# Performance work log

Hardware: AMD Instinct MI355X
Metric: run time of the kernel (lower is better)

Reference implementation:

```python
import jax, jax.numpy as jnp
import numpy as np

B, SP, SH, H, E, V, C = 128, 128, 64, 1024, 300, 50000, 4


def setup_inputs() -> dict:
    key = jax.random.key(0)
    ks = jax.random.split(key, 21)
    def n(k, shape, sc=0.05):
        return sc * jax.random.normal(k, shape, dtype=jnp.float32)
    return {
        "premise": jax.random.randint(ks[0], (B, SP), 0, V),
        "hypothesis": jax.random.randint(ks[1], (B, SH), 0, V),
        "emb": n(ks[2], (V, E), 1.0),
        "w_ih_p": n(ks[3], (4 * H, E)), "w_hh_p": n(ks[4], (4 * H, H)),
        "b_ih_p": n(ks[5], (4 * H,)), "b_hh_p": n(ks[6], (4 * H,)),
        "w_ih_h": n(ks[7], (4 * H, E)), "w_hh_h": n(ks[8], (4 * H, H)),
        "b_ih_h": n(ks[9], (4 * H,)), "b_hh_h": n(ks[10], (4 * H,)),
        "wy": n(ks[11], (H, H)), "wh": n(ks[12], (H, H)), "wr": n(ks[13], (H, H)),
        "w": n(ks[14], (H, 1)), "wt": n(ks[15], (H, H)),
        "wp": n(ks[16], (H, H)), "wx": n(ks[17], (H, H)),
        "fc_w": n(ks[18], (C, H)), "fc_b": n(ks[19], (C,)),
    }


def _lstm(x_seq, h0, c0, w_ih, w_hh, b_ih, b_hh):
    # x_seq: [S, B, E]; PyTorch LSTMCell gate order i, f, g, o
    def step(carry, x):
        h, c = carry
        g = x @ w_ih.T + b_ih + h @ w_hh.T + b_hh
        i, f, gg, o = jnp.split(g, 4, axis=-1)
        c2 = jax.nn.sigmoid(f) * c + jax.nn.sigmoid(i) * jnp.tanh(gg)
        h2 = jax.nn.sigmoid(o) * jnp.tanh(c2)
        return (h2, c2), (h2, c2)
    _, (hs, cs) = jax.lax.scan(step, (h0, c0), x_seq)
    return hs, cs  # [S, B, H]


def _mask_carry(seq, init, m):
    # seq: [S,B,H], m: [S,B,1]; carry last valid value through padded steps
    def step(prev, xm):
        x, mt = xm
        cur = mt * x + (1.0 - mt) * prev
        return cur, cur
    last, out = jax.lax.scan(step, init, (seq, m))
    return out, last


def _forward(premise, hypothesis, emb, w_ih_p, w_hh_p, b_ih_p, b_hh_p,
             w_ih_h, w_hh_h, b_ih_h, b_hh_h, wy, wh, wr, w, wt, wp, wx, fc_w, fc_b):
    x_p = emb[premise]                                   # [B,SP,E]
    x_h = emb[hypothesis]                                # [B,SH,E]
    m_p = (premise != 0).astype(jnp.float32)             # [B,SP]
    m_h = (hypothesis != 0).astype(jnp.float32)          # [B,SH]
    Bsz, Hh = premise.shape[0], w_hh_p.shape[1]
    h0 = jnp.zeros((Bsz, Hh), jnp.float32)
    c0 = jnp.zeros((Bsz, Hh), jnp.float32)

    # premise LSTM (runs through pads, outputs masked afterwards, as in torch)
    hs_p, cs_p = _lstm(jnp.swapaxes(x_p, 0, 1), h0, c0, w_ih_p, w_hh_p, b_ih_p, b_hh_p)
    mp_s = jnp.swapaxes(m_p, 0, 1)[:, :, None]           # [SP,B,1]
    out_p, _ = _mask_carry(hs_p, h0, mp_s)
    _, c_last = _mask_carry(cs_p, c0, mp_s)              # masked cell_p[:, -1, :]

    # hypothesis LSTM initialized with (h0, masked last premise cell)
    hs_h, _ = _lstm(jnp.swapaxes(x_h, 0, 1), h0, c_last, w_ih_h, w_hh_h, b_ih_h, b_hh_h)
    mh_s = jnp.swapaxes(m_h, 0, 1)[:, :, None]           # [SH,B,1]
    out_h, out_h_last = _mask_carry(hs_h, h0, mh_s)      # [SH,B,H], [B,H]

    # word-by-word attention over premise at each hypothesis step
    Y = jnp.swapaxes(out_p, 0, 1)                        # [B,SP,H]
    first = jnp.einsum('bph,hk->bpk', Y, wy)             # hoisted: constant over steps
    neg = -1000.0 * (1.0 - m_p)                          # [B,SP]

    def att_step(r, hm):
        h_t, mt = hm                                     # [B,H], [B,1]
        second = h_t @ wh + r @ wr
        M = jnp.tanh(first + second[:, None, :])         # [B,SP,H]
        alpha = jax.nn.softmax(jnp.squeeze(M @ w, -1) + neg, axis=1)
        r_t = jnp.einsum('bp,bph->bh', alpha, Y) + jnp.tanh(r @ wt)
        r_t = mt * r_t + (1.0 - mt) * r
        return r_t, None

    r_last, _ = jax.lax.scan(att_step, jnp.zeros((Bsz, Hh), jnp.float32), (out_h, mh_s))

    h_star = jnp.tanh(r_last @ wp + out_h_last @ wx)
    logits = h_star @ fc_w.T + fc_b
    # eval mode: dropout is identity, softmax output
    return jax.nn.softmax(logits, axis=1)


def reference(premise, hypothesis, emb, w_ih_p, w_hh_p, b_ih_p, b_hh_p,
              w_ih_h, w_hh_h, b_ih_h, b_hh_h, wy, wh, wr, w, wt, wp, wx, fc_w, fc_b):
    return _forward(premise, hypothesis, emb, w_ih_p, w_hh_p, b_ih_p, b_hh_p,
                    w_ih_h, w_hh_h, b_ih_h, b_hh_h, wy, wh, wr, w, wt, wp, wx, fc_w, fc_b)
```

## Files before the change

kernel.cpp:

```cpp
#include <hip/hip_runtime.h>


using u16 = unsigned short;
using u32 = unsigned int;
using u64 = unsigned long long;
typedef short bf16x8 __attribute__((ext_vector_type(8)));
typedef float f32x4 __attribute__((ext_vector_type(4)));

constexpr int B  = 128;
constexpr int SP = 128;
constexpr int SH = 64;
constexpr int H  = 1024;
constexpr int E  = 300;
constexpr int NC = 4;
constexpr int G4H  = 4 * H;
constexpr int EPAD = 320;
constexpr int KCAT = EPAD + H;
constexpr int NB_L = 256;
constexpr int NB_A = 256;
constexpr size_t BHE = (size_t)B * H;

__device__ __forceinline__ float sigf(float x) { return 1.0f / (1.0f + __expf(-x)); }
__device__ __forceinline__ float tanh_fast(float x) {
    float e = __expf(2.0f * x);
    return 1.0f - 2.0f / (e + 1.0f);
}
__device__ __forceinline__ u16 f2bf(float x) {
    union { float f; unsigned u; } v; v.f = x;
    unsigned r = v.u + 0x7fffu + ((v.u >> 16) & 1u);
    return (u16)(r >> 16);
}
__device__ __forceinline__ float bf2f(u16 h) {
    union { unsigned u; float f; } v; v.u = ((unsigned)h) << 16;
    return v.f;
}
__device__ __forceinline__ f32x4 mfma16(bf16x8 a, bf16x8 b, f32x4 c) {
    return __builtin_amdgcn_mfma_f32_16x16x32_bf16(a, b, c, 0, 0, 0);
}
__device__ __forceinline__ u32 packhl(float v) {
    u16 hi = f2bf(v);
    u16 lo = f2bf(v - bf2f(hi));
    return ((u32)hi << 16) | lo;
}

__device__ __forceinline__ float aLdF(const float* p) {
    return __hip_atomic_load(p, __ATOMIC_RELAXED, __HIP_MEMORY_SCOPE_AGENT);
}
__device__ __forceinline__ void aStF(float* p, float v) {
    __hip_atomic_store(p, v, __ATOMIC_RELAXED, __HIP_MEMORY_SCOPE_AGENT);
}
__device__ __forceinline__ void aSt32(u32* p, u32 v) {
    __hip_atomic_store(p, v, __ATOMIC_RELAXED, __HIP_MEMORY_SCOPE_AGENT);
}
__device__ __forceinline__ void aSt64(u64* p, u64 v) {
    __hip_atomic_store(p, v, __ATOMIC_RELAXED, __HIP_MEMORY_SCOPE_AGENT);
}

__device__ __forceinline__ void flag_arrive(int* flags, int epoch) {
    asm volatile("s_waitcnt vmcnt(0)" ::: "memory");
    __syncthreads();
    if (threadIdx.x == 0)
        __hip_atomic_store(&flags[blockIdx.x], epoch,
                           __ATOMIC_RELAXED, __HIP_MEMORY_SCOPE_AGENT);
}
__device__ __forceinline__ void flag_wait(int* flags, int n, int epoch) {
    for (;;) {
        int v = (threadIdx.x < n)
            ? __hip_atomic_load(&flags[threadIdx.x], __ATOMIC_RELAXED,
                                __HIP_MEMORY_SCOPE_AGENT)
            : epoch;
        if (__syncthreads_and(v >= epoch)) break;
        __builtin_amdgcn_s_sleep(8);
    }
    asm volatile("" ::: "memory");
    __builtin_amdgcn_sched_barrier(0);
}

__global__ __launch_bounds__(256)
void wcat_split_kernel(const float* __restrict__ w_ih, const float* __restrict__ w_hh,
                       u16* __restrict__ dh, u16* __restrict__ dl)
{
    int col = blockIdx.x * 256 + threadIdx.x;
    int n = blockIdx.y;
    if (col >= KCAT) return;
    float v = 0.f;
    if (col < E)          v = w_ih[(size_t)n * E + col];
    else if (col >= EPAD) v = w_hh[(size_t)n * H + (col - EPAD)];
    u16 hi = f2bf(v);
    dh[(size_t)n * KCAT + col] = hi;
    dl[(size_t)n * KCAT + col] = f2bf(v - bf2f(hi));
}

__global__ __launch_bounds__(256)
void tsplit_kernel(const float* __restrict__ src, u16* __restrict__ dh, u16* __restrict__ dl)
{
    int k = blockIdx.x * 256 + threadIdx.x;
    int n = blockIdx.y;
    float v = src[(size_t)k * H + n];
    u16 hi = f2bf(v);
    dh[(size_t)n * H + k] = hi;
    dl[(size_t)n * H + k] = f2bf(v - bf2f(hi));
}

__global__ __launch_bounds__(256)
void wrt_split_kernel(const float* __restrict__ wr, const float* __restrict__ wt,
                      u16* __restrict__ dh, u16* __restrict__ dl)
{
    int k = blockIdx.x * 256 + threadIdx.x;
    int n = blockIdx.y;
    float v = (n < H) ? wr[(size_t)k * H + n] : wt[(size_t)k * H + (n - H)];
    u16 hi = f2bf(v);
    dh[(size_t)n * H + k] = hi;
    dl[(size_t)n * H + k] = f2bf(v - bf2f(hi));
}

template<int PREMISE>
__global__ __launch_bounds__(256, 1)
void lstm_scan(const int* __restrict__ toks, int S,
               const float* __restrict__ emb,
               const u16* __restrict__ Wh, const u16* __restrict__ Wl,
               const float* __restrict__ b_ih, const float* __restrict__ b_hh,
               const u32* __restrict__ h0,
               u32* __restrict__ hseq,
               float* __restrict__ c, float* __restrict__ hmask,
               float* __restrict__ cmask,
               u16* __restrict__ seq_hi, u16* __restrict__ seq_lo,
               int* __restrict__ flags)
{
    const int tid  = threadIdx.x;
    const int lane = tid & 63;
    const int g    = tid >> 6;
    const int l15  = lane & 15;
    const int lk8  = (lane >> 4) * 8;
    const int bx   = blockIdx.x & 63;
    const int by   = blockIdx.x >> 6;
    const int k0   = bx * 16;
    const int m0   = by * 32;

    bf16x8 wh_r[42], wl_r[42];
    {
        const u16* ph = Wh + (size_t)(g * H + k0 + l15) * KCAT + lk8;
        const u16* pl = Wl + (size_t)(g * H + k0 + l15) * KCAT + lk8;
#pragma unroll
        for (int ks = 0; ks < 42; ++ks) {
            wh_r[ks] = *(const bf16x8*)(ph + ks * 32);
            wl_r[ks] = *(const bf16x8*)(pl + ks * 32);
        }
    }
    const int ke = k0 + (tid & 15);
    const float bs0 = b_ih[0 * H + ke] + b_hh[0 * H + ke];
    const float bs1 = b_ih[1 * H + ke] + b_hh[1 * H + ke];
    const float bs2 = b_ih[2 * H + ke] + b_hh[2 * H + ke];
    const float bs3 = b_ih[3 * H + ke] + b_hh[3 * H + ke];

    __shared__ u16 hiL[32][1032];
    __shared__ u16 loL[32][1032];
    __shared__ float gt[4][32][17];

    for (int t = 0; t < S; ++t) {
        const u32* hin = (t == 0) ? h0 : (hseq + (size_t)(t - 1) * BHE);
        u32*      hout = hseq + (size_t)t * BHE;

        const float* ea[2];
#pragma unroll
        for (int mt = 0; mt < 2; ++mt) {
            int row = m0 + mt * 16 + l15;
            int tok = toks[row * S + t];
            ea[mt] = emb + (size_t)tok * E + lk8;
        }

        f32x4 acc[2] = {{0.f,0.f,0.f,0.f},{0.f,0.f,0.f,0.f}};

#pragma unroll
        for (int ks = 0; ks < 9; ++ks) {
#pragma unroll
            for (int mt = 0; mt < 2; ++mt) {
                float4 f0 = *(const float4*)(ea[mt] + ks * 32);
                float4 f1 = *(const float4*)(ea[mt] + ks * 32 + 4);
                float v[8] = {f0.x, f0.y, f0.z, f0.w, f1.x, f1.y, f1.z, f1.w};
                bf16x8 a_hi, a_lo;
#pragma unroll
                for (int j = 0; j < 8; ++j) {
                    u16 hi = f2bf(v[j]);
                    a_hi[j] = (short)hi;
                    a_lo[j] = (short)f2bf(v[j] - bf2f(hi));
                }
                acc[mt] = mfma16(a_hi, wh_r[ks], acc[mt]);
                acc[mt] = mfma16(a_lo, wh_r[ks], acc[mt]);
                acc[mt] = mfma16(a_hi, wl_r[ks], acc[mt]);
            }
        }
        {
#pragma unroll
            for (int mt = 0; mt < 2; ++mt) {
                float v[8];
#pragma unroll
                for (int j = 0; j < 8; ++j) {
                    int k = 288 + lk8 + j;
                    v[j] = (k < E) ? ea[mt][k - lk8] : 0.f;
                }
                bf16x8 a_hi, a_lo;
#pragma unroll
                for (int j = 0; j < 8; ++j) {
                    u16 hi = f2bf(v[j]);
                    a_hi[j] = (short)hi;
                    a_lo[j] = (short)f2bf(v[j] - bf2f(hi));
                }
                acc[mt] = mfma16(a_hi, wh_r[9], acc[mt]);
                acc[mt] = mfma16(a_lo, wh_r[9], acc[mt]);
                acc[mt] = mfma16(a_hi, wl_r[9], acc[mt]);
            }
        }

        if (t > 0) flag_wait(flags, NB_L, t);

        {
            const u64* hsrc = (const u64*)(hin + (size_t)m0 * H);
#pragma unroll 16
            for (int j = 0; j < 64; ++j) {
                int i = j * 256 + tid;
                u64 v = hsrc[i];
                u32 p0 = (u32)v, p1 = (u32)(v >> 32);
                int row = i >> 9, cp = (i & 511) * 2;
                *(u32*)&hiL[row][cp] = (p0 >> 16) | (p1 & 0xffff0000u);
                *(u32*)&loL[row][cp] = (p0 & 0xffffu) | (p1 << 16);
            }
        }
        __syncthreads();

#pragma unroll
        for (int ks = 0; ks < 32; ++ks) {
#pragma unroll
            for (int mt = 0; mt < 2; ++mt) {
                bf16x8 a_hi = *(const bf16x8*)&hiL[mt * 16 + l15][ks * 32 + lk8];
                bf16x8 a_lo = *(const bf16x8*)&loL[mt * 16 + l15][ks * 32 + lk8];
                acc[mt] = mfma16(a_hi, wh_r[10 + ks], acc[mt]);
                acc[mt] = mfma16(a_lo, wh_r[10 + ks], acc[mt]);
                acc[mt] = mfma16(a_hi, wl_r[10 + ks], acc[mt]);
            }
        }
        __syncthreads();

#pragma unroll
        for (int mt = 0; mt < 2; ++mt)
#pragma unroll
            for (int j = 0; j < 4; ++j)
                gt[g][mt * 16 + (lane >> 4) * 4 + j][l15] = acc[mt][j];
        __syncthreads();

#pragma unroll
        for (int i = 0; i < 2; ++i) {
            int ml = (tid >> 4) + i * 16;
            int m  = m0 + ml;
            size_t idx = (size_t)m * H + ke;
            float gi = gt[0][ml][tid & 15] + bs0;
            float gf = gt[1][ml][tid & 15] + bs1;
            float gg = gt[2][ml][tid & 15] + bs2;
            float go = gt[3][ml][tid & 15] + bs3;
            float c2 = sigf(gf) * c[idx] + sigf(gi) * tanh_fast(gg);
            float h2 = sigf(go) * tanh_fast(c2);
            c[idx] = c2;
            aSt32(&hout[idx], packhl(h2));
            float mk = (toks[m * S + t] != 0) ? 1.f : 0.f;
            float hmv = mk * h2 + (1.f - mk) * hmask[idx];
            hmask[idx] = hmv;
            u16 mh = f2bf(hmv);
            u16 mlv = f2bf(hmv - bf2f(mh));
            if (PREMISE) {
                float cmv = mk * c2 + (1.f - mk) * cmask[idx];
                cmask[idx] = cmv;
                size_t yi = ((size_t)m * SP + t) * H + ke;
                seq_hi[yi] = mh; seq_lo[yi] = mlv;
            } else {
                size_t oi = ((size_t)t * B + m) * H + ke;
                seq_hi[oi] = mh; seq_lo[oi] = mlv;
            }
        }
        if (t + 1 < S) flag_arrive(flags, t + 1);
    }
}

__global__ __launch_bounds__(256, 1)
void attn_scan(const u16* __restrict__ firstH, const u16* __restrict__ firstL,
               const u16* __restrict__ hsecH, const u16* __restrict__ hsecL,
               const u16* __restrict__ Wrth, const u16* __restrict__ Wrtl,
               const u16* __restrict__ Yh, const u16* __restrict__ Yl,
               const float* __restrict__ wv,
               const int* __restrict__ ptoks, const int* __restrict__ htoks,
               float* __restrict__ srt,
               float* __restrict__ sglob,
               u32* __restrict__ rseq,
               float* __restrict__ r,
               int* __restrict__ flags)
{
    const int tid  = threadIdx.x;
    const int lane = tid & 63;
    const int w    = tid >> 6;
    const int l15  = lane & 15;
    const int lk8  = (lane >> 4) * 8;
    const int b    = blockIdx.x >> 1;
    const int sub  = blockIdx.x & 1;

    __shared__ u16 rs_hi[16][1032];
    __shared__ u16 rs_lo[16][1032];
    __shared__ float al[SP];
    __shared__ float red[SP];

    float wv_e[16];
#pragma unroll
    for (int e = 0; e < 16; ++e) wv_e[e] = wv[lane + e * 64];

    const int pm0 = (blockIdx.x >> 5) * 16;
    const int n0  = (((blockIdx.x & 31) << 2) + w) * 16;
    const ptrdiff_t dB = Wrtl - Wrth;

    for (int t = 0; t < SH; ++t) {
        {
            const u64* rsrc = (const u64*)(rseq + (size_t)t * BHE + (size_t)pm0 * H);
#pragma unroll 16
            for (int j = 0; j < 32; ++j) {
                int i = j * 256 + tid;
                u64 v = rsrc[i];
                u32 p0 = (u32)v, p1 = (u32)(v >> 32);
                int row = i >> 9, cp = (i & 511) * 2;
                *(u32*)&rs_hi[row][cp] = (p0 >> 16) | (p1 & 0xffff0000u);
                *(u32*)&rs_lo[row][cp] = (p0 & 0xffffu) | (p1 << 16);
            }
        }
        __syncthreads();

        {
            const u16* bp0 = Wrth + (size_t)(n0 + l15) * H + lk8;
            f32x4 a0 = {0.f,0.f,0.f,0.f};
#pragma unroll 4
            for (int ks = 0; ks < 32; ++ks) {
                bf16x8 ahi = *(const bf16x8*)&rs_hi[l15][ks * 32 + lk8];
                bf16x8 alo = *(const bf16x8*)&rs_lo[l15][ks * 32 + lk8];
                bf16x8 b0h = *(const bf16x8*)(bp0 + ks * 32);
                bf16x8 b0l = *(const bf16x8*)(bp0 + dB + ks * 32);
                a0 = mfma16(ahi, b0h, a0);
                a0 = mfma16(alo, b0h, a0);
                a0 = mfma16(ahi, b0l, a0);
            }
#pragma unroll
            for (int j = 0; j < 4; ++j) {
                int mrow = pm0 + (lane >> 4) * 4 + j;
                aStF(&srt[(size_t)mrow * 2048 + n0 + l15], a0[j]);
            }
        }
        flag_arrive(flags, 3 * t + 1);
        flag_wait(flags, NB_A, 3 * t + 1);

        {
            float hsum[16];
            const u16* hbh = hsecH + ((size_t)t * B + b) * H;
            const u16* hbl = hsecL + ((size_t)t * B + b) * H;
            const float* sb = srt + (size_t)b * 2048;
#pragma unroll
            for (int e = 0; e < 16; ++e) {
                int hh = lane + e * 64;
                hsum[e] = bf2f(hbh[hh]) + bf2f(hbl[hh]) + aLdF(&sb[hh]);
            }
            for (int pp = 0; pp < 16; ++pp) {
                int p = sub * 64 + w * 16 + pp;
                const u16* fph = firstH + ((size_t)b * SP + p) * H;
                const u16* fpl = firstL + ((size_t)b * SP + p) * H;
                float acc = 0.f;
#pragma unroll
                for (int e = 0; e < 16; ++e) {
                    int hh = lane + e * 64;
                    acc += tanh_fast(bf2f(fph[hh]) + bf2f(fpl[hh]) + hsum[e]) * wv_e[e];
                }
#pragma unroll
                for (int off = 32; off; off >>= 1) acc += __shfl_xor(acc, off);
                if (lane == 0)
                    aStF(&sglob[b * SP + p],
                         acc + ((ptoks[b * SP + p] != 0) ? 0.f : -1000.f));
            }
        }
        flag_arrive(flags, 3 * t + 2);
        flag_wait(flags, NB_A, 3 * t + 2);

        {
            if (tid < SP) { float v = aLdF(&sglob[b * SP + tid]); al[tid] = v; red[tid] = v; }
            __syncthreads();
            for (int off = 64; off; off >>= 1) {
                if (tid < off) red[tid] = fmaxf(red[tid], red[tid + off]);
                __syncthreads();
            }
            float mx = red[0];
            __syncthreads();
            if (tid < SP) { float e = __expf(al[tid] - mx); al[tid] = e; red[tid] = e; }
            __syncthreads();
            for (int off = 64; off; off >>= 1) {
                if (tid < off) red[tid] += red[tid + off];
                __syncthreads();
            }
            float inv = 1.f / red[0];
            __syncthreads();
            if (tid < SP) al[tid] *= inv;
            __syncthreads();

            const int c0 = sub * 512 + tid * 2;
            const u16* ybh = Yh + (size_t)b * SP * H + c0;
            const u16* ybl = Yl + (size_t)b * SP * H + c0;
            float a0 = 0.f, a1 = 0.f, b0 = 0.f, b1 = 0.f;
#pragma unroll 8
            for (int p = 0; p < SP; ++p) {
                float a = al[p];
                u32 vh = *(const u32*)(ybh + (size_t)p * H);
                u32 vl = *(const u32*)(ybl + (size_t)p * H);
                float e0 = __uint_as_float(vh << 16) + __uint_as_float(vl << 16);
                float e1 = __uint_as_float(vh & 0xffff0000u) + __uint_as_float(vl & 0xffff0000u);
                if (p & 1) { b0 += a * e0; b1 += a * e1; }
                else       { a0 += a * e0; a1 += a * e1; }
            }
            a0 += b0; a1 += b1;
            float mk = (htoks[b * SH + t] != 0) ? 1.f : 0.f;
            float rwt0 = aLdF(&srt[(size_t)b * 2048 + H + c0]);
            float rwt1 = aLdF(&srt[(size_t)b * 2048 + H + c0 + 1]);
            float ro0 = r[(size_t)b * H + c0];
            float ro1 = r[(size_t)b * H + c0 + 1];
            float rn0 = a0 + tanh_fast(rwt0);
            float rn1 = a1 + tanh_fast(rwt1);
            float rv0 = mk * rn0 + (1.f - mk) * ro0;
            float rv1 = mk * rn1 + (1.f - mk) * ro1;
            r[(size_t)b * H + c0]     = rv0;
            r[(size_t)b * H + c0 + 1] = rv1;
            u32 pk0 = packhl(rv0), pk1 = packhl(rv1);
            aSt64((u64*)(rseq + (size_t)(t + 1) * BHE + (size_t)b * H + c0),
                  ((u64)pk1 << 32) | pk0);
        }
        if (t + 1 < SH) {
            flag_arrive(flags, 3 * t + 3);
            flag_wait(flags, NB_A, 3 * t + 3);
        }
    }
}

template<bool SPLITOUT>
__global__ __launch_bounds__(256)
void gemm_mfma_kernel(const u16* __restrict__ Ah, const u16* __restrict__ Al,
                      const u16* __restrict__ Bh, const u16* __restrict__ Bl,
                      float* __restrict__ C, u16* __restrict__ Ch, u16* __restrict__ Cl,
                      int M, int N, int K)
{
    const int tid  = threadIdx.x;
    const int lane = tid & 63;
    const int wave = tid >> 6;
    const int l15  = lane & 15;
    const int lk8  = (lane >> 4) * 8;
    const int m0   = blockIdx.y * 64 + wave * 16;
    const int n0   = blockIdx.x * 64;

    const u16* ahp = Ah + (size_t)(m0 + l15) * K + lk8;
    const u16* alp = Al + (size_t)(m0 + l15) * K + lk8;
    const u16* bhp[4]; const u16* blp[4];
#pragma unroll
    for (int nt = 0; nt < 4; ++nt) {
        size_t o = (size_t)(n0 + nt * 16 + l15) * K + lk8;
        bhp[nt] = Bh + o; blp[nt] = Bl + o;
    }
    f32x4 acc[4] = {{0.f,0.f,0.f,0.f},{0.f,0.f,0.f,0.f},
                    {0.f,0.f,0.f,0.f},{0.f,0.f,0.f,0.f}};
    const int nks = K >> 5;
#pragma unroll 2
    for (int ks = 0; ks < nks; ++ks) {
        bf16x8 a_hi = *(const bf16x8*)(ahp + ks * 32);
        bf16x8 a_lo = *(const bf16x8*)(alp + ks * 32);
#pragma unroll
        for (int nt = 0; nt < 4; ++nt) {
            bf16x8 b_hi = *(const bf16x8*)(bhp[nt] + ks * 32);
            bf16x8 b_lo = *(const bf16x8*)(blp[nt] + ks * 32);
            acc[nt] = mfma16(a_hi, b_hi, acc[nt]);
            acc[nt] = mfma16(a_lo, b_hi, acc[nt]);
            acc[nt] = mfma16(a_hi, b_lo, acc[nt]);
        }
    }
#pragma unroll
    for (int nt = 0; nt < 4; ++nt)
#pragma unroll
        for (int j = 0; j < 4; ++j) {
            int m = m0 + (lane >> 4) * 4 + j;
            size_t idx = (size_t)m * N + n0 + nt * 16 + l15;
            if (SPLITOUT) {
                float v = acc[nt][j];
                u16 hi = f2bf(v);
                Ch[idx] = hi;
                Cl[idx] = f2bf(v - bf2f(hi));
            } else {
                C[idx] = acc[nt][j];
            }
        }
}

template<bool ACC>
__global__ __launch_bounds__(256)
void skinny_kernel(const float* __restrict__ A,
                   const float* __restrict__ B1, float* __restrict__ C1,
                   const float* __restrict__ B2, float* __restrict__ C2,
                   int K, int N, int ntiles)
{
    const int tid = threadIdx.x;
    const int tx = tid & 15, ty = tid >> 4;
    const int bx = blockIdx.x;
    const float* Bw = (bx < ntiles) ? B1 : B2;
    float* C       = (bx < ntiles) ? C1 : C2;
    const int n0 = ((bx < ntiles) ? bx : bx - ntiles) * 64;
    const int m0 = blockIdx.y * 32;

    __shared__ float As[2][16][34];
    __shared__ float Bs[2][16][68];
    const int sq = tid & 15, sm = tid >> 4;
    const int nb = tid & 63, kb = tid >> 6;

    float ra[2], rb[4];
    auto ldA = [&](int k0, int rr) -> float {
        return A[(size_t)(m0 + sm + 16 * rr) * K + k0 + sq];
    };
    auto ldB = [&](int k0, int rr) -> float {
        return Bw[(size_t)(k0 + kb + 4 * rr) * N + n0 + nb];
    };

    float acc[2][4] = {};
    ra[0] = ldA(0, 0); ra[1] = ldA(0, 1);
#pragma unroll
    for (int rr = 0; rr < 4; ++rr) rb[rr] = ldB(0, rr);
    As[0][sq][sm] = ra[0]; As[0][sq][sm + 16] = ra[1];
#pragma unroll
    for (int rr = 0; rr < 4; ++rr) Bs[0][kb + 4 * rr][nb] = rb[rr];
    __syncthreads();

    const int NKT = K / 16;
    for (int kt = 0; kt < NKT; ++kt) {
        const int buf = kt & 1;
        if (kt + 1 < NKT) {
            int k0 = (kt + 1) * 16;
            ra[0] = ldA(k0, 0); ra[1] = ldA(k0, 1);
#pragma unroll
            for (int rr = 0; rr < 4; ++rr) rb[rr] = ldB(k0, rr);
        }
#pragma unroll
        for (int qq = 0; qq < 16; ++qq) {
            float2 a2 = *(const float2*)&As[buf][qq][ty * 2];
            float4 b4 = *(const float4*)&Bs[buf][qq][tx * 4];
            acc[0][0] += a2.x * b4.x; acc[0][1] += a2.x * b4.y;
            acc[0][2] += a2.x * b4.z; acc[0][3] += a2.x * b4.w;
            acc[1][0] += a2.y * b4.x; acc[1][1] += a2.y * b4.y;
            acc[1][2] += a2.y * b4.z; acc[1][3] += a2.y * b4.w;
        }
        if (kt + 1 < NKT) {
            const int nbuf = buf ^ 1;
            As[nbuf][sq][sm] = ra[0]; As[nbuf][sq][sm + 16] = ra[1];
#pragma unroll
            for (int rr = 0; rr < 4; ++rr) Bs[nbuf][kb + 4 * rr][nb] = rb[rr];
            __syncthreads();
        }
    }
#pragma unroll
    for (int i = 0; i < 2; ++i) {
        int m = m0 + ty * 2 + i;
        float* cp = &C[(size_t)m * N + n0 + tx * 4];
        float4 v = make_float4(acc[i][0], acc[i][1], acc[i][2], acc[i][3]);
        if (ACC) {
            float4 o = *(const float4*)cp;
            v.x += o.x; v.y += o.y; v.z += o.z; v.w += o.w;
        }
        *(float4*)cp = v;
    }
}

__global__ __launch_bounds__(256)
void final_kernel(const float* __restrict__ pre,
                  const float* __restrict__ fc_w,
                  const float* __restrict__ fc_b,
                  float* __restrict__ out)
{
    int b = blockIdx.x;
    float acc[NC] = {0.f, 0.f, 0.f, 0.f};
    for (int k = threadIdx.x; k < H; k += 256) {
        float hs = tanh_fast(pre[(size_t)b * H + k]);
#pragma unroll
        for (int cc = 0; cc < NC; ++cc) acc[cc] += hs * fc_w[cc * H + k];
    }
    __shared__ float red[NC][256];
#pragma unroll
    for (int cc = 0; cc < NC; ++cc) red[cc][threadIdx.x] = acc[cc];
    __syncthreads();
    for (int off = 128; off > 0; off >>= 1) {
        if (threadIdx.x < off)
#pragma unroll
            for (int cc = 0; cc < NC; ++cc)
                red[cc][threadIdx.x] += red[cc][threadIdx.x + off];
        __syncthreads();
    }
    if (threadIdx.x == 0) {
        float l[NC], mx = -1e30f;
#pragma unroll
        for (int cc = 0; cc < NC; ++cc) { l[cc] = red[cc][0] + fc_b[cc]; mx = fmaxf(mx, l[cc]); }
        float sum = 0.f;
#pragma unroll
        for (int cc = 0; cc < NC; ++cc) { l[cc] = __expf(l[cc] - mx); sum += l[cc]; }
#pragma unroll
        for (int cc = 0; cc < NC; ++cc) out[b * NC + cc] = l[cc] / sum;
    }
}

extern "C" void kernel_launch(void* const* d_in, const int* in_sizes, int n_in,
                              void* d_out, int out_size, void* d_ws, size_t ws_size,
                              hipStream_t stream)
{
    const int*   prem   = (const int*)d_in[0];
    const int*   hyp    = (const int*)d_in[1];
    const float* emb    = (const float*)d_in[2];
    const float* w_ih_p = (const float*)d_in[3];
    const float* w_hh_p = (const float*)d_in[4];
    const float* b_ih_p = (const float*)d_in[5];
    const float* b_hh_p = (const float*)d_in[6];
    const float* w_ih_h = (const float*)d_in[7];
    const float* w_hh_h = (const float*)d_in[8];
    const float* b_ih_h = (const float*)d_in[9];
    const float* b_hh_h = (const float*)d_in[10];
    const float* wy     = (const float*)d_in[11];
    const float* wh     = (const float*)d_in[12];
    const float* wr     = (const float*)d_in[13];
    const float* wv     = (const float*)d_in[14];
    const float* wt     = (const float*)d_in[15];
    const float* wp     = (const float*)d_in[16];
    const float* wx     = (const float*)d_in[17];
    const float* fc_w   = (const float*)d_in[18];
    const float* fc_b   = (const float*)d_in[19];
    float* out = (float*)d_out;
    (void)in_sizes; (void)n_in; (void)out_size; (void)ws_size;

    char* wsc = (char*)d_ws;
    size_t off = 0;
    auto alloc = [&](size_t bytes) -> void* {
        void* p = wsc + off;
        off += (bytes + 255) & ~(size_t)255;
        return p;
    };
    constexpr size_t WSZ = (size_t)G4H * KCAT * 2;
    constexpr size_t SLAB = BHE * 4;

    char* regionA = (char*)alloc(4 * WSZ);
    u16* Wp_hi = (u16*)regionA;
    u16* Wp_lo = (u16*)(regionA + WSZ);
    u16* Wq_hi = (u16*)(regionA + 2 * WSZ);
    u16* Wq_lo = (u16*)(regionA + 3 * WSZ);
    u32* rseq  = (u32*)regionA;

    u16* wyT_hi = (u16*)alloc((size_t)H * H * 2);
    u16* wyT_lo = (u16*)alloc((size_t)H * H * 2);
    u16* whT_hi = (u16*)alloc((size_t)H * H * 2);
    u16* whT_lo = (u16*)alloc((size_t)H * H * 2);
    u16* WrtH   = (u16*)alloc((size_t)2 * H * H * 2);
    u16* WrtL   = (u16*)alloc((size_t)2 * H * H * 2);

    u16* Y_hi   = (u16*)alloc((size_t)B * SP * H * 2);
    u16* Y_lo   = (u16*)alloc((size_t)B * SP * H * 2);

    char* regionE = (char*)alloc((size_t)SP * SLAB);
    u32* hseqP  = (u32*)regionE;
    u16* OH_hi  = (u16*)regionE;
    u16* OH_lo  = (u16*)(regionE + (size_t)SH * B * H * 2);
    u16* firstH = (u16*)regionE;
    u16* firstL = (u16*)(regionE + (size_t)B * SP * H * 2);

    char* regionF = (char*)alloc((size_t)SH * SLAB);
    u32* hseqH = (u32*)regionF;
    u16* hsecH = (u16*)regionF;
    u16* hsecL = (u16*)(regionF + (size_t)SH * B * H * 2);

    u32* h0zero = (u32*)alloc(SLAB);
    float* cbuf = (float*)alloc(SLAB);
    float* hm   = (float*)alloc(SLAB);
    float* cm   = (float*)alloc(SLAB);
    float* r    = (float*)alloc(SLAB);
    float* srt  = (float*)alloc((size_t)B * 2048 * 4);
    float* sglob= (float*)alloc((size_t)B * SP * 4);
    float* pre  = (float*)alloc(SLAB);
    int*   bars = (int*)alloc(3 * 256 * sizeof(int));
    int* barP = bars; int* barH = bars + 256; int* barA = bars + 512;

    dim3 gW((KCAT + 255) / 256, G4H);
    wcat_split_kernel<<<gW, 256, 0, stream>>>(w_ih_p, w_hh_p, Wp_hi, Wp_lo);
    wcat_split_kernel<<<gW, 256, 0, stream>>>(w_ih_h, w_hh_h, Wq_hi, Wq_lo);
    tsplit_kernel<<<dim3(H / 256, H), 256, 0, stream>>>(wy, wyT_hi, wyT_lo);
    tsplit_kernel<<<dim3(H / 256, H), 256, 0, stream>>>(wh, whT_hi, whT_lo);
    wrt_split_kernel<<<dim3(H / 256, 2 * H), 256, 0, stream>>>(wr, wt, WrtH, WrtL);

    hipMemsetAsync(h0zero, 0, SLAB, stream);
    hipMemsetAsync(cbuf, 0, 3 * SLAB, stream);
    hipMemsetAsync(bars, 0, 3 * 256 * sizeof(int), stream);

    lstm_scan<1><<<NB_L, 256, 0, stream>>>(
        prem, SP, emb, Wp_hi, Wp_lo, b_ih_p, b_hh_p,
        h0zero, hseqP, cbuf, hm, cm, Y_hi, Y_lo, barP);

    hipMemsetAsync(hm, 0, SLAB, stream);
    lstm_scan<0><<<NB_L, 256, 0, stream>>>(
        hyp, SH, emb, Wq_hi, Wq_lo, b_ih_h, b_hh_h,
        h0zero, hseqH, cm, hm, (float*)nullptr, OH_hi, OH_lo, barH);

    gemm_mfma_kernel<true><<<dim3(H / 64, (SH * B) / 64), 256, 0, stream>>>(
        OH_hi, OH_lo, whT_hi, whT_lo, nullptr, hsecH, hsecL, SH * B, H, H);
    gemm_mfma_kernel<true><<<dim3(H / 64, (B * SP) / 64), 256, 0, stream>>>(
        Y_hi, Y_lo, wyT_hi, wyT_lo, nullptr, firstH, firstL, B * SP, H, H);

    hipMemsetAsync(rseq, 0, SLAB, stream);
    hipMemsetAsync(r, 0, SLAB, stream);
    attn_scan<<<NB_A, 256, 0, stream>>>(
        firstH, firstL, hsecH, hsecL, WrtH, WrtL, Y_hi, Y_lo, wv, prem, hyp,
        srt, sglob, rseq, r, barA);

    skinny_kernel<false><<<dim3(16, 4), 256, 0, stream>>>(r,  wp, pre, nullptr, nullptr, H, H, 16);
    skinny_kernel<true ><<<dim3(16, 4), 256, 0, stream>>>(hm, wx, pre, nullptr, nullptr, H, H, 16);
    final_kernel<<<B, 256, 0, stream>>>(pre, fc_w, fc_b, out);
}
```

Measured before the change: 11.07 ms.

## Use group-local barriers, interleaved hi/lo packing, and double attention grid

Replaces the global all-block flag barriers in the LSTM and attention scans with barriers scoped to groups of 64 blocks, plus a 4-block barrier per batch row for the softmax step. This cuts cross-block synchronization latency on each step. Stores the bf16 hi/lo split pairs interleaved into one u32 array so each element needs one load instead of two. The attention grid grows from 256 to 512 blocks, and each block does half the score and context work. The risk is correctness if a group barrier misses a real cross-group dependency, and 512 blocks must all be co-resident for the spin waits to avoid deadlock.

```diff
diff --git a/kernel.cpp b/kernel.cpp
--- a/kernel.cpp
+++ b/kernel.cpp
@@ -17,7 +17,7 @@
 constexpr int EPAD = 320;
 constexpr int KCAT = EPAD + H;
 constexpr int NB_L = 256;
-constexpr int NB_A = 256;
+constexpr int NB_A = 512;
 constexpr size_t BHE = (size_t)B * H;
 
 __device__ __forceinline__ float sigf(float x) { return 1.0f / (1.0f + __expf(-x)); }
@@ -34,6 +34,10 @@
     union { unsigned u; float f; } v; v.u = ((unsigned)h) << 16;
     return v.f;
 }
+__device__ __forceinline__ float uaf(u32 u) { return __uint_as_float(u); }
+__device__ __forceinline__ float unpk(u32 v) {
+    return uaf(v & 0xffff0000u) + uaf(v << 16);
+}
 __device__ __forceinline__ f32x4 mfma16(bf16x8 a, bf16x8 b, f32x4 c) {
     return __builtin_amdgcn_mfma_f32_16x16x32_bf16(a, b, c, 0, 0, 0);
 }
@@ -56,21 +60,21 @@
     __hip_atomic_store(p, v, __ATOMIC_RELAXED, __HIP_MEMORY_SCOPE_AGENT);
 }
 
-__device__ __forceinline__ void flag_arrive(int* flags, int epoch) {
+__device__ __forceinline__ void grp_arrive(int* flags, int epoch) {
     asm volatile("s_waitcnt vmcnt(0)" ::: "memory");
     __syncthreads();
     if (threadIdx.x == 0)
         __hip_atomic_store(&flags[blockIdx.x], epoch,
                            __ATOMIC_RELAXED, __HIP_MEMORY_SCOPE_AGENT);
 }
-__device__ __forceinline__ void flag_wait(int* flags, int n, int epoch) {
+__device__ __forceinline__ void grp_wait(int* flags, int base, int n, int epoch) {
     for (;;) {
         int v = (threadIdx.x < n)
-            ? __hip_atomic_load(&flags[threadIdx.x], __ATOMIC_RELAXED,
-                                __HIP_MEMORY_SCOPE_AGENT)
+            ? __hip_atomic_load(&flags[base + (int)threadIdx.x],
+                                __ATOMIC_RELAXED, __HIP_MEMORY_SCOPE_AGENT)
             : epoch;
         if (__syncthreads_and(v >= epoch)) break;
-        __builtin_amdgcn_s_sleep(8);
+        __builtin_amdgcn_s_sleep(4);
     }
     asm volatile("" ::: "memory");
     __builtin_amdgcn_sched_barrier(0);
@@ -124,7 +128,7 @@
                u32* __restrict__ hseq,
                float* __restrict__ c, float* __restrict__ hmask,
                float* __restrict__ cmask,
-               u16* __restrict__ seq_hi, u16* __restrict__ seq_lo,
+               u32* __restrict__ seq_pk,
                int* __restrict__ flags)
 {
     const int tid  = threadIdx.x;
@@ -136,6 +140,7 @@
     const int by   = blockIdx.x >> 6;
     const int k0   = bx * 16;
     const int m0   = by * 32;
+    const int gbase = by * 64;
 
     bf16x8 wh_r[42], wl_r[42];
     {
@@ -212,7 +217,7 @@
             }
         }
 
-        if (t > 0) flag_wait(flags, NB_L, t);
+        if (t > 0) grp_wait(flags, gbase, 64, t);
 
         {
             const u64* hsrc = (const u64*)(hin + (size_t)m0 * H);
@@ -266,52 +271,56 @@
             hmask[idx] = hmv;
             u16 mh = f2bf(hmv);
             u16 mlv = f2bf(hmv - bf2f(mh));
+            u32 pk = ((u32)mh << 16) | mlv;
             if (PREMISE) {
                 float cmv = mk * c2 + (1.f - mk) * cmask[idx];
                 cmask[idx] = cmv;
-                size_t yi = ((size_t)m * SP + t) * H + ke;
-                seq_hi[yi] = mh; seq_lo[yi] = mlv;
+                seq_pk[((size_t)m * SP + t) * H + ke] = pk;
             } else {
-                size_t oi = ((size_t)t * B + m) * H + ke;
-                seq_hi[oi] = mh; seq_lo[oi] = mlv;
-            }
-        }
-        if (t + 1 < S) flag_arrive(flags, t + 1);
+                seq_pk[((size_t)t * B + m) * H + ke] = pk;
+            }
+        }
+        if (t + 1 < S) grp_arrive(flags, t + 1);
     }
 }
 
 __global__ __launch_bounds__(256, 1)
-void attn_scan(const u16* __restrict__ firstH, const u16* __restrict__ firstL,
-               const u16* __restrict__ hsecH, const u16* __restrict__ hsecL,
+void attn_scan(const u32* __restrict__ first_pk,
+               const u32* __restrict__ hsec_pk,
                const u16* __restrict__ Wrth, const u16* __restrict__ Wrtl,
-               const u16* __restrict__ Yh, const u16* __restrict__ Yl,
+               const u32* __restrict__ Ypk,
                const float* __restrict__ wv,
                const int* __restrict__ ptoks, const int* __restrict__ htoks,
                float* __restrict__ srt,
                float* __restrict__ sglob,
                u32* __restrict__ rseq,
                float* __restrict__ r,
-               int* __restrict__ flags)
+               int* __restrict__ gflags, int* __restrict__ sflags)
 {
     const int tid  = threadIdx.x;
     const int lane = tid & 63;
     const int w    = tid >> 6;
     const int l15  = lane & 15;
     const int lk8  = (lane >> 4) * 8;
-    const int b    = blockIdx.x >> 1;
-    const int sub  = blockIdx.x & 1;
+    const int b    = blockIdx.x >> 2;
+    const int sub  = blockIdx.x & 3;
+    const int grp  = blockIdx.x >> 6;
+    const int gbase = grp * 64;
+    const int ig   = blockIdx.x & 63;
+    const int sbase = b * 4;
 
     __shared__ u16 rs_hi[16][1032];
     __shared__ u16 rs_lo[16][1032];
     __shared__ float al[SP];
     __shared__ float red[SP];
+    __shared__ float ps[128][2];
 
     float wv_e[16];
 #pragma unroll
     for (int e = 0; e < 16; ++e) wv_e[e] = wv[lane + e * 64];
 
-    const int pm0 = (blockIdx.x >> 5) * 16;
-    const int n0  = (((blockIdx.x & 31) << 2) + w) * 16;
+    const int pm0 = grp * 16;
+    const int n0  = (ig * 2 + w) * 16;
     const ptrdiff_t dB = Wrtl - Wrth;
 
     for (int t = 0; t < SH; ++t) {
@@ -329,7 +338,7 @@
         }
         __syncthreads();
 
-        {
+        if (w < 2) {
             const u16* bp0 = Wrth + (size_t)(n0 + l15) * H + lk8;
             f32x4 a0 = {0.f,0.f,0.f,0.f};
 #pragma unroll 4
@@ -348,29 +357,25 @@
                 aStF(&srt[(size_t)mrow * 2048 + n0 + l15], a0[j]);
             }
         }
-        flag_arrive(flags, 3 * t + 1);
-        flag_wait(flags, NB_A, 3 * t + 1);
+        grp_arrive(gflags, 2 * t + 1);
+        grp_wait(gflags, gbase, 64, 2 * t + 1);
 
         {
             float hsum[16];
-            const u16* hbh = hsecH + ((size_t)t * B + b) * H;
-            const u16* hbl = hsecL + ((size_t)t * B + b) * H;
+            const u32* hpk = hsec_pk + ((size_t)t * B + b) * H;
             const float* sb = srt + (size_t)b * 2048;
 #pragma unroll
             for (int e = 0; e < 16; ++e) {
                 int hh = lane + e * 64;
-                hsum[e] = bf2f(hbh[hh]) + bf2f(hbl[hh]) + aLdF(&sb[hh]);
-            }
-            for (int pp = 0; pp < 16; ++pp) {
-                int p = sub * 64 + w * 16 + pp;
-                const u16* fph = firstH + ((size_t)b * SP + p) * H;
-                const u16* fpl = firstL + ((size_t)b * SP + p) * H;
+                hsum[e] = unpk(hpk[hh]) + aLdF(&sb[hh]);
+            }
+            for (int pp = 0; pp < 8; ++pp) {
+                int p = sub * 32 + w * 8 + pp;
+                const u32* fpk = first_pk + ((size_t)b * SP + p) * H;
                 float acc = 0.f;
 #pragma unroll
-                for (int e = 0; e < 16; ++e) {
-                    int hh = lane + e * 64;
-                    acc += tanh_fast(bf2f(fph[hh]) + bf2f(fpl[hh]) + hsum[e]) * wv_e[e];
-                }
+                for (int e = 0; e < 16; ++e)
+                    acc += tanh_fast(unpk(fpk[lane + e * 64]) + hsum[e]) * wv_e[e];
 #pragma unroll
                 for (int off = 32; off; off >>= 1) acc += __shfl_xor(acc, off);
                 if (lane == 0)
@@ -378,8 +383,8 @@
                          acc + ((ptoks[b * SP + p] != 0) ? 0.f : -1000.f));
             }
         }
-        flag_arrive(flags, 3 * t + 2);
-        flag_wait(flags, NB_A, 3 * t + 2);
+        grp_arrive(sflags, t + 1);
+        grp_wait(sflags, sbase, 4, t + 1);
 
         {
             if (tid < SP) { float v = aLdF(&sglob[b * SP + tid]); al[tid] = v; red[tid] = v; }
@@ -401,49 +406,47 @@
             if (tid < SP) al[tid] *= inv;
             __syncthreads();
 
-            const int c0 = sub * 512 + tid * 2;
-            const u16* ybh = Yh + (size_t)b * SP * H + c0;
-            const u16* ybl = Yl + (size_t)b * SP * H + c0;
-            float a0 = 0.f, a1 = 0.f, b0 = 0.f, b1 = 0.f;
-#pragma unroll 8
-            for (int p = 0; p < SP; ++p) {
+            const int half = tid >> 7;
+            const int tl   = tid & 127;
+            const int c0   = sub * 256 + tl * 2;
+            const u32* yp = Ypk + (size_t)b * SP * H + c0;
+            float s0 = 0.f, s1 = 0.f;
+#pragma unroll 4
+            for (int pp = 0; pp < 64; ++pp) {
+                int p = half * 64 + pp;
                 float a = al[p];
-                u32 vh = *(const u32*)(ybh + (size_t)p * H);
-                u32 vl = *(const u32*)(ybl + (size_t)p * H);
-                float e0 = __uint_as_float(vh << 16) + __uint_as_float(vl << 16);
-                float e1 = __uint_as_float(vh & 0xffff0000u) + __uint_as_float(vl & 0xffff0000u);
-                if (p & 1) { b0 += a * e0; b1 += a * e1; }
-                else       { a0 += a * e0; a1 += a * e1; }
-            }
-            a0 += b0; a1 += b1;
-            float mk = (htoks[b * SH + t] != 0) ? 1.f : 0.f;
-            float rwt0 = aLdF(&srt[(size_t)b * 2048 + H + c0]);
-            float rwt1 = aLdF(&srt[(size_t)b * 2048 + H + c0 + 1]);
-            float ro0 = r[(size_t)b * H + c0];
-            float ro1 = r[(size_t)b * H + c0 + 1];
-            float rn0 = a0 + tanh_fast(rwt0);
-            float rn1 = a1 + tanh_fast(rwt1);
-            float rv0 = mk * rn0 + (1.f - mk) * ro0;
-            float rv1 = mk * rn1 + (1.f - mk) * ro1;
-            r[(size_t)b * H + c0]     = rv0;
-            r[(size_t)b * H + c0 + 1] = rv1;
-            u32 pk0 = packhl(rv0), pk1 = packhl(rv1);
-            aSt64((u64*)(rseq + (size_t)(t + 1) * BHE + (size_t)b * H + c0),
-                  ((u64)pk1 << 32) | pk0);
+                u64 v = *(const u64*)(yp + (size_t)p * H);
+                s0 += a * unpk((u32)v);
+                s1 += a * unpk((u32)(v >> 32));
+            }
+            if (half) { ps[tl][0] = s0; ps[tl][1] = s1; }
+            __syncthreads();
+            if (!half) {
+                s0 += ps[tl][0]; s1 += ps[tl][1];
+                float mk = (htoks[b * SH + t] != 0) ? 1.f : 0.f;
+                float rn0 = s0 + tanh_fast(aLdF(&srt[(size_t)b * 2048 + H + c0]));
+                float rn1 = s1 + tanh_fast(aLdF(&srt[(size_t)b * 2048 + H + c0 + 1]));
+                float ro0 = r[(size_t)b * H + c0];
+                float ro1 = r[(size_t)b * H + c0 + 1];
+                float rv0 = mk * rn0 + (1.f - mk) * ro0;
+                float rv1 = mk * rn1 + (1.f - mk) * ro1;
+                r[(size_t)b * H + c0]     = rv0;
+                r[(size_t)b * H + c0 + 1] = rv1;
+                aSt64((u64*)(rseq + (size_t)(t + 1) * BHE + (size_t)b * H + c0),
+                      ((u64)packhl(rv1) << 32) | packhl(rv0));
+            }
         }
         if (t + 1 < SH) {
-            flag_arrive(flags, 3 * t + 3);
-            flag_wait(flags, NB_A, 3 * t + 3);
-        }
-    }
-}
-
-template<bool SPLITOUT>
+            grp_arrive(gflags, 2 * t + 2);
+            grp_wait(gflags, gbase, 64, 2 * t + 2);
+        }
+    }
+}
+
 __global__ __launch_bounds__(256)
-void gemm_mfma_kernel(const u16* __restrict__ Ah, const u16* __restrict__ Al,
-                      const u16* __restrict__ Bh, const u16* __restrict__ Bl,
-                      float* __restrict__ C, u16* __restrict__ Ch, u16* __restrict__ Cl,
-                      int M, int N, int K)
+void gemm_pk_kernel(const u32* __restrict__ Apk,
+                    const u16* __restrict__ Bh, const u16* __restrict__ Bl,
+                    u32* __restrict__ Cpk, int M, int N, int K)
 {
     const int tid  = threadIdx.x;
     const int lane = tid & 63;
@@ -453,8 +456,7 @@
     const int m0   = blockIdx.y * 64 + wave * 16;
     const int n0   = blockIdx.x * 64;
 
-    const u16* ahp = Ah + (size_t)(m0 + l15) * K + lk8;
-    const u16* alp = Al + (size_t)(m0 + l15) * K + lk8;
+    const u32* ap = Apk + (size_t)(m0 + l15) * K + lk8;
     const u16* bhp[4]; const u16* blp[4];
 #pragma unroll
     for (int nt = 0; nt < 4; ++nt) {
@@ -466,8 +468,15 @@
     const int nks = K >> 5;
 #pragma unroll 2
     for (int ks = 0; ks < nks; ++ks) {
-        bf16x8 a_hi = *(const bf16x8*)(ahp + ks * 32);
-        bf16x8 a_lo = *(const bf16x8*)(alp + ks * 32);
+        uint4 v0 = *(const uint4*)(ap + ks * 32);
+        uint4 v1 = *(const uint4*)(ap + ks * 32 + 4);
+        u32 vv[8] = {v0.x, v0.y, v0.z, v0.w, v1.x, v1.y, v1.z, v1.w};
+        bf16x8 a_hi, a_lo;
+#pragma unroll
+        for (int j = 0; j < 8; ++j) {
+            a_hi[j] = (short)(vv[j] >> 16);
+            a_lo[j] = (short)(vv[j] & 0xffffu);
+        }
 #pragma unroll
         for (int nt = 0; nt < 4; ++nt) {
             bf16x8 b_hi = *(const bf16x8*)(bhp[nt] + ks * 32);
@@ -482,15 +491,7 @@
 #pragma unroll
         for (int j = 0; j < 4; ++j) {
             int m = m0 + (lane >> 4) * 4 + j;
-            size_t idx = (size_t)m * N + n0 + nt * 16 + l15;
-            if (SPLITOUT) {
-                float v = acc[nt][j];
-                u16 hi = f2bf(v);
-                Ch[idx] = hi;
-                Cl[idx] = f2bf(v - bf2f(hi));
-            } else {
-                C[idx] = acc[nt][j];
-            }
+            Cpk[(size_t)m * N + n0 + nt * 16 + l15] = packhl(acc[nt][j]);
         }
 }
 
@@ -657,20 +658,16 @@
     u16* WrtH   = (u16*)alloc((size_t)2 * H * H * 2);
     u16* WrtL   = (u16*)alloc((size_t)2 * H * H * 2);
 
-    u16* Y_hi   = (u16*)alloc((size_t)B * SP * H * 2);
-    u16* Y_lo   = (u16*)alloc((size_t)B * SP * H * 2);
+    u32* Ypk = (u32*)alloc((size_t)B * SP * H * 4);
 
     char* regionE = (char*)alloc((size_t)SP * SLAB);
-    u32* hseqP  = (u32*)regionE;
-    u16* OH_hi  = (u16*)regionE;
-    u16* OH_lo  = (u16*)(regionE + (size_t)SH * B * H * 2);
-    u16* firstH = (u16*)regionE;
-    u16* firstL = (u16*)(regionE + (size_t)B * SP * H * 2);
+    u32* hseqP    = (u32*)regionE;
+    u32* OHpk     = (u32*)regionE;
+    u32* first_pk = (u32*)regionE;
 
     char* regionF = (char*)alloc((size_t)SH * SLAB);
-    u32* hseqH = (u32*)regionF;
-    u16* hsecH = (u16*)regionF;
-    u16* hsecL = (u16*)(regionF + (size_t)SH * B * H * 2);
+    u32* hseqH   = (u32*)regionF;
+    u32* hsec_pk = (u32*)regionF;
 
     u32* h0zero = (u32*)alloc(SLAB);
     float* cbuf = (float*)alloc(SLAB);
@@ -680,8 +677,10 @@
     float* srt  = (float*)alloc((size_t)B * 2048 * 4);
     float* sglob= (float*)alloc((size_t)B * SP * 4);
     float* pre  = (float*)alloc(SLAB);
-    int*   bars = (int*)alloc(3 * 256 * sizeof(int));
-    int* barP = bars; int* barH = bars + 256; int* barA = bars + 512;
+    int* barP   = (int*)alloc(256 * sizeof(int));
+    int* barH   = (int*)alloc(256 * sizeof(int));
+    int* gflA   = (int*)alloc(512 * sizeof(int));
+    int* sflA   = (int*)alloc(512 * sizeof(int));
 
     dim3 gW((KCAT + 255) / 256, G4H);
     wcat_split_kernel<<<gW, 256, 0, stream>>>(w_ih_p, w_hh_p, Wp_hi, Wp_lo);
@@ -692,27 +691,30 @@
 
     hipMemsetAsync(h0zero, 0, SLAB, stream);
     hipMemsetAsync(cbuf, 0, 3 * SLAB, stream);
-    hipMemsetAsync(bars, 0, 3 * 256 * sizeof(int), stream);
+    hipMemsetAsync(barP, 0, 256 * sizeof(int), stream);
+    hipMemsetAsync(barH, 0, 256 * sizeof(int), stream);
+    hipMemsetAsync(gflA, 0, 512 * sizeof(int), stream);
+    hipMemsetAsync(sflA, 0, 512 * sizeof(int), stream);
 
     lstm_scan<1><<<NB_L, 256, 0, stream>>>(
         prem, SP, emb, Wp_hi, Wp_lo, b_ih_p, b_hh_p,
-        h0zero, hseqP, cbuf, hm, cm, Y_hi, Y_lo, barP);
+        h0zero, hseqP, cbuf, hm, cm, Ypk, barP);
 
     hipMemsetAsync(hm, 0, SLAB, stream);
     lstm_scan<0><<<NB_L, 256, 0, stream>>>(
         hyp, SH, emb, Wq_hi, Wq_lo, b_ih_h, b_hh_h,
-        h0zero, hseqH, cm, hm, (float*)nullptr, OH_hi, OH_lo, barH);
-
-    gemm_mfma_kernel<true><<<dim3(H / 64, (SH * B) / 64), 256, 0, stream>>>(
-        OH_hi, OH_lo, whT_hi, whT_lo, nullptr, hsecH, hsecL, SH * B, H, H);
-    gemm_mfma_kernel<true><<<dim3(H / 64, (B * SP) / 64), 256, 0, stream>>>(
-        Y_hi, Y_lo, wyT_hi, wyT_lo, nullptr, firstH, firstL, B * SP, H, H);
+        h0zero, hseqH, cm, hm, (float*)nullptr, OHpk, barH);
+
+    gemm_pk_kernel<<<dim3(H / 64, (SH * B) / 64), 256, 0, stream>>>(
+        OHpk, whT_hi, whT_lo, hsec_pk, SH * B, H, H);
+    gemm_pk_kernel<<<dim3(H / 64, (B * SP) / 64), 256, 0, stream>>>(
+        Ypk, wyT_hi, wyT_lo, first_pk, B * SP, H, H);
 
     hipMemsetAsync(rseq, 0, SLAB, stream);
     hipMemsetAsync(r, 0, SLAB, stream);
     attn_scan<<<NB_A, 256, 0, stream>>>(
-        firstH, firstL, hsecH, hsecL, WrtH, WrtL, Y_hi, Y_lo, wv, prem, hyp,
-        srt, sglob, rseq, r, barA);
+        first_pk, hsec_pk, WrtH, WrtL, Ypk, wv, prem, hyp,
+        srt, sglob, rseq, r, gflA, sflA);
 
     skinny_kernel<false><<<dim3(16, 4), 256, 0, stream>>>(r,  wp, pre, nullptr, nullptr, H, H, 16);
     skinny_kernel<true ><<<dim3(16, 4), 256, 0, stream>>>(hm, wx, pre, nullptr, nullptr, H, H, 16);
```

Result: faster. 10.31 ms (-6.8%).
